# Kernel optimization log

Hardware: AMD Instinct MI355X
Metric: run time of the kernel (lower is better)

The kernel has to match this reference:

```python
import jax, jax.numpy as jnp
from jax import lax
import numpy as np

IMG = 512
NUM_CLASSES = 80
K_PRE = 256            # per-class pre-NMS candidates (TF combined NMS prunes similarly)
MAX_PER_CLASS = 100
MAX_TOTAL = 100
IOU_THR = 0.5
ANY_IOU_THR = 0.7
SCORE_THR = 0.05
NEG = -1e9


def make_anchors(img=IMG):
    """RetinaNet-style anchors for FPN levels 3..7, 9 per cell, [y1,x1,y2,x2]."""
    out = []
    for l in range(3, 8):
        s = 2 ** l
        n = img // s
        c = (np.arange(n) + 0.5) * s
        cy, cx = np.meshgrid(c, c, indexing='ij')
        base = 4.0 * s
        hs, ws = [], []
        for r in [0.5, 1.0, 2.0]:
            for sc in [1.0, 2 ** (1 / 3), 2 ** (2 / 3)]:
                hs.append(base * sc * np.sqrt(r))
                ws.append(base * sc / np.sqrt(r))
        hs = np.asarray(hs); ws = np.asarray(ws)  # [9]
        cy = cy[..., None]; cx = cx[..., None]
        a = np.stack([cy - hs / 2, cx - ws / 2, cy + hs / 2, cx + ws / 2], -1)  # [n,n,9,4]
        out.append(a.reshape(-1, 4))
    return np.concatenate(out, 0).astype(np.float32)


def setup_inputs() -> dict:
    key = jax.random.key(0)
    k1, k2, k3, k4 = jax.random.split(key, 4)
    anchors = jnp.asarray(make_anchors())          # [49104, 4]
    A = anchors.shape[0]
    B = 8
    # logits biased low, mimicking focal-loss bias init; few anchors fire
    y_cls = jax.random.normal(k1, (B, A, NUM_CLASSES), jnp.float32) - 4.0
    y_bbox = jax.random.normal(k2, (B, A, 4), jnp.float32) * 0.1
    orig_hs = jax.random.randint(k3, (B,), 480, 1080).astype(jnp.int32)
    orig_ws = jax.random.randint(k4, (B,), 640, 1920).astype(jnp.int32)
    return {"y_cls": y_cls, "y_bbox": y_bbox, "anchors": anchors,
            "orig_hs": orig_hs, "orig_ws": orig_ws}


def decode_boxes(anchors, rel):
    """bboxes_from_fast_rcnn: anchors [A,4], rel [B,A,4] -> [B,A,4] (y1,x1,y2,x2)."""
    ha = anchors[:, 2] - anchors[:, 0]
    wa = anchors[:, 3] - anchors[:, 1]
    cya = anchors[:, 0] + 0.5 * ha
    cxa = anchors[:, 1] + 0.5 * wa
    cy = cya + rel[..., 0] * ha
    cx = cxa + rel[..., 1] * wa
    h = ha * jnp.exp(rel[..., 2])
    w = wa * jnp.exp(rel[..., 3])
    return jnp.stack([cy - 0.5 * h, cx - 0.5 * w, cy + 0.5 * h, cx + 0.5 * w], -1)


def pairwise_iou(b):
    """[K,4] -> [K,K] IoU."""
    y1, x1, y2, x2 = b[:, 0], b[:, 1], b[:, 2], b[:, 3]
    area = (y2 - y1) * (x2 - x1)
    ih = jnp.maximum(jnp.minimum(y2[:, None], y2[None, :]) - jnp.maximum(y1[:, None], y1[None, :]), 0.0)
    iw = jnp.maximum(jnp.minimum(x2[:, None], x2[None, :]) - jnp.maximum(x1[:, None], x1[None, :]), 0.0)
    inter = ih * iw
    return inter / (area[:, None] + area[None, :] - inter + 1e-8)


def greedy_nms(boxes, valid, iou_thr, max_keep):
    """Greedy NMS over score-sorted boxes [K,4]; returns keep mask [K]."""
    K = boxes.shape[0]
    iou_m = pairwise_iou(boxes)
    ar = jnp.arange(K)

    def step(sup, i):
        k = valid[i] & jnp.logical_not(sup[i])
        sup = sup | (k & (iou_m[i] > iou_thr) & (ar > i))
        return sup, k

    _, keep = lax.scan(step, jnp.zeros(K, bool), ar)
    rank = jnp.cumsum(keep) - 1
    return keep & (rank < max_keep)


def reference(y_cls, y_bbox, anchors, orig_hs, orig_ws):
    B, A, C = y_cls.shape
    scores = jax.nn.sigmoid(y_cls)                 # [B,A,C]
    boxes = decode_boxes(anchors, y_bbox)          # [B,A,4]

    # --- per-class combined NMS ---
    st = jnp.swapaxes(scores, 1, 2)                # [B,C,A]
    top_s, top_i = lax.top_k(st, K_PRE)            # [B,C,K]
    boxes_c = jnp.take_along_axis(boxes[:, None, :, :], top_i[..., None], axis=2)  # [B,C,K,4]
    valid = top_s > SCORE_THR
    keep = jax.vmap(jax.vmap(lambda b, v: greedy_nms(b, v, IOU_THR, MAX_PER_CLASS)))(boxes_c, valid)

    masked = jnp.where(keep, top_s, NEG).reshape(B, -1)           # [B,C*K]
    cls_ids = jnp.broadcast_to(jnp.arange(C, dtype=jnp.float32)[None, :, None],
                               (B, C, K_PRE)).reshape(B, -1)
    boxes_flat = boxes_c.reshape(B, -1, 4)

    sel_s, sel_i = lax.top_k(masked, MAX_TOTAL)    # [B,T]
    sel_valid = sel_s > NEG / 2
    sel_boxes = jnp.take_along_axis(boxes_flat, sel_i[..., None], axis=1)
    sel_cls = jnp.take_along_axis(cls_ids, sel_i, axis=1)
    out_scores = jnp.where(sel_valid, sel_s, 0.0)
    out_boxes = jnp.where(sel_valid[..., None], sel_boxes, 0.0)
    out_cls = jnp.where(sel_valid, sel_cls, 0.0)
    valid_det = jnp.sum(sel_valid, axis=1).astype(jnp.int32)

    # --- resize to original image dims (bboxes_resize) ---
    rh = orig_hs.astype(jnp.float32) / IMG
    rw = orig_ws.astype(jnp.float32) / IMG
    scale = jnp.stack([rh, rw, rh, rw], -1)[:, None, :]
    lim = jnp.stack([orig_hs, orig_ws, orig_hs, orig_ws], -1).astype(jnp.float32)[:, None, :]
    rb = jnp.clip(out_boxes * scale, 0.0, lim)

    # --- class-agnostic second NMS (scores already sorted desc) ---
    v2 = jnp.arange(MAX_TOTAL)[None, :] < valid_det[:, None]
    keep2 = jax.vmap(lambda b, v: greedy_nms(b, v, ANY_IOU_THR, MAX_TOTAL))(rb, v2)

    # compact kept detections to the front (ragged gather in the original)
    perm = jnp.argsort(jnp.logical_not(keep2), axis=1, stable=True)
    fb = jnp.take_along_axis(rb, perm[..., None], axis=1)
    fs = jnp.take_along_axis(out_scores, perm, axis=1)
    fc = jnp.take_along_axis(out_cls, perm, axis=1)
    nv = jnp.sum(keep2, axis=1).astype(jnp.int32)
    m = jnp.arange(MAX_TOTAL)[None, :] < nv[:, None]
    return (jnp.where(m[..., None], fb, 0.0), jnp.where(m, fs, 0.0), jnp.where(m, fc, 0.0), nv)
```

## Files before the change

### kernel.cpp

```cpp
#include <hip/hip_runtime.h>
#include <cstdint>

#define NEGF    (-1.0e9f)
#define THR_PRE (-1.55f)
#define THR_VALID (-2.9444389791664403f)
#define CAP 512
#define FCAP 1024
#define NCLS 80
#define APB 372
#define BCAP 512
#define BLCAP 8192

__device__ __forceinline__ unsigned fkey(float v){
  unsigned b = __float_as_uint(v);
  return b ^ ((b & 0x80000000u) ? 0xFFFFFFFFu : 0x80000000u);
}
__device__ __forceinline__ float fkey_inv(unsigned k){
  unsigned b = (k & 0x80000000u) ? (k ^ 0x80000000u) : ~k;
  return __uint_as_float(b);
}

template<int N, int NT>
__device__ void bitonic_desc(unsigned long long* buf){
  const int tid = threadIdx.x;
  __syncthreads();
  for (int k = 2; k <= N; k <<= 1){
    for (int j = k >> 1; j > 0; j >>= 1){
      for (int t = tid; t < N/2; t += NT){
        int i = ((t & ~(j-1)) << 1) | (t & (j-1));
        int p = i | j;
        unsigned long long a = buf[i], b = buf[p];
        bool sw = ((i & k) == 0) ? (a < b) : (a > b);
        if (sw){ buf[i] = b; buf[p] = a; }
      }
      __syncthreads();
    }
  }
}

__global__ void k_init(unsigned* cnt, int n, unsigned* bcnt, int nb){
  int i = blockIdx.x*blockDim.x + threadIdx.x;
  if (i < n) cnt[i] = 0u;
  if (i < nb) bcnt[i] = 0u;
}

__global__ void k_filter(const float* __restrict__ ycls, int A,
                         unsigned* __restrict__ cnt, unsigned long long* __restrict__ pairs){
  const int b  = blockIdx.y;
  const int a0 = blockIdx.x * APB;
  const int tid = threadIdx.x;
  __shared__ unsigned long long s_cand[BCAP];
  __shared__ unsigned char     s_crow[BCAP];
  __shared__ unsigned s_n;
  __shared__ unsigned s_cnt[NCLS], s_base[NCLS], s_cur[NCLS];
  if (tid == 0) s_n = 0;
  if (tid < NCLS){ s_cnt[tid] = 0u; s_cur[tid] = 0u; }
  __syncthreads();

  const float4* p4 = (const float4*)(ycls + ((size_t)b*A + a0)*NCLS);
  const int nval = (min(APB, A - a0)) * NCLS;
  const int n4 = nval >> 2;
  for (int t = tid; t < n4; t += blockDim.x){
    float4 v = p4[t];
    int idx  = t << 2;
    int aloc = idx / NCLS;
    int c0   = idx - aloc*NCLS;
    unsigned a = (unsigned)(a0 + aloc);
    float vv[4] = {v.x, v.y, v.z, v.w};
    #pragma unroll
    for (int j = 0; j < 4; j++){
      if (vv[j] > THR_PRE){
        unsigned s = atomicAdd(&s_n, 1u);
        if (s < BCAP){
          s_cand[s] = ((unsigned long long)fkey(vv[j]) << 32) | (unsigned)(~a);
          s_crow[s] = (unsigned char)(c0 + j);
        }
      }
    }
  }
  __syncthreads();
  unsigned n = s_n; if (n > BCAP) n = BCAP;
  for (unsigned i = tid; i < n; i += blockDim.x)
    atomicAdd(&s_cnt[s_crow[i]], 1u);
  __syncthreads();
  if (tid < NCLS && s_cnt[tid] > 0u)
    s_base[tid] = atomicAdd(&cnt[b*NCLS + tid], s_cnt[tid]);
  __syncthreads();
  for (unsigned i = tid; i < n; i += blockDim.x){
    int c = s_crow[i];
    unsigned off = s_base[c] + atomicAdd(&s_cur[c], 1u);
    if (off < CAP) pairs[(size_t)(b*NCLS + c)*CAP + off] = s_cand[i];
  }
}

__global__ void k_topk_nms(const unsigned* __restrict__ cnt, const unsigned long long* __restrict__ pairs,
                           const float* __restrict__ ycls, const float4* __restrict__ ybbox,
                           const float4* __restrict__ anchors,
                           float4* __restrict__ sbox,
                           unsigned long long* __restrict__ bcand, unsigned* __restrict__ bcnt,
                           unsigned A, unsigned C){
  const int row = blockIdx.x, tid = threadIdx.x;
  const unsigned b = (unsigned)row / C, c = (unsigned)row % C;
  __shared__ __align__(16) char smem[5120];
  unsigned long long* L = (unsigned long long*)smem;
  __shared__ unsigned s_n;
  __shared__ unsigned long long s_K;
  __shared__ unsigned long long s_keep[4];
  __shared__ unsigned s_kc, s_bbase;

  unsigned long long a, bb;
  unsigned n = cnt[row]; if (n > CAP) n = CAP;
  if (n >= 256u){
    const unsigned long long* pr = pairs + (size_t)row*CAP;
    int i0 = 2*tid, i1 = 2*tid + 1;
    a  = (i0 < (int)n) ? pr[i0] : 0ull;
    bb = (i1 < (int)n) ? pr[i1] : 0ull;
  } else {
    if (tid == 0) s_n = 0;
    __syncthreads();
    for (int i = tid; i < CAP; i += 256) L[i] = 0ull;
    __syncthreads();
    for (unsigned aa = tid; aa < A; aa += 256){
      float v = ycls[((size_t)b*A + aa)*C + c];
      if (v > THR_VALID){
        unsigned s = atomicAdd(&s_n, 1u);
        if (s < CAP) L[s] = ((unsigned long long)fkey(v) << 32) | (unsigned)(~aa);
      }
    }
    __syncthreads();
    n = s_n; if (n > CAP) n = CAP;
    a = L[2*tid]; bb = L[2*tid + 1];
    __syncthreads();
  }

  auto ce_local = [&](int k){
    bool desc = (((2*tid) & k) == 0);
    bool sw = desc ? (a < bb) : (a > bb);
    if (sw){ unsigned long long t = a; a = bb; bb = t; }
  };
  auto ce_shfl = [&](int k, int m){
    unsigned long long pa = __shfl_xor(a, m);
    unsigned long long pb = __shfl_xor(bb, m);
    bool low  = ((tid & m) == 0);
    bool desc = (((2*tid) & k) == 0);
    bool takeMax = (low == desc);
    a  = takeMax ? (a  > pa ? a  : pa) : (a  < pa ? a  : pa);
    bb = takeMax ? (bb > pb ? bb : pb) : (bb < pb ? bb : pb);
  };
  auto ce_lds = [&](int k, int j){
    L[2*tid] = a; L[2*tid + 1] = bb;
    __syncthreads();
    unsigned long long pa = L[(2*tid) ^ j];
    unsigned long long pb = L[(2*tid + 1) ^ j];
    bool lowa = (((2*tid) & j) == 0);
    bool desc = (((2*tid) & k) == 0);
    bool takeMax = (lowa == desc);
    a  = takeMax ? (a  > pa ? a  : pa) : (a  < pa ? a  : pa);
    bb = takeMax ? (bb > pb ? bb : pb) : (bb < pb ? bb : pb);
    __syncthreads();
  };

  ce_local(2);
  #pragma unroll
  for (int k = 4; k <= 128; k <<= 1){
    #pragma unroll
    for (int m = k >> 2; m >= 1; m >>= 1) ce_shfl(k, m);
    ce_local(k);
  }
  ce_lds(256, 128);
  #pragma unroll
  for (int m = 32; m >= 1; m >>= 1) ce_shfl(256, m);
  ce_local(256);
  ce_lds(512, 256);
  ce_lds(512, 128);
  #pragma unroll
  for (int m = 32; m >= 1; m >>= 1) ce_shfl(512, m);
  ce_local(512);

  if (tid < 128){ L[2*tid] = a; L[2*tid + 1] = bb; }
  __syncthreads();
  unsigned long long p = L[tid];
  __syncthreads();

  unsigned m = n < 256u ? n : 256u;
  float lg = NEGF; float4 bx = make_float4(0.f,0.f,0.f,0.f);
  if ((unsigned)tid < m){
    unsigned key = (unsigned)(p >> 32);
    unsigned aidx = ~(unsigned)(p & 0xFFFFFFFFull);
    lg = fkey_inv(key);
    float4 an = anchors[aidx];
    float4 rl = ybbox[(size_t)b*A + aidx];
    float ha = an.z - an.x, wa = an.w - an.y;
    float cya = an.x + 0.5f*ha, cxa = an.y + 0.5f*wa;
    float cy = cya + rl.x*ha, cx = cxa + rl.y*wa;
    float h = ha * expf(rl.z), w = wa * expf(rl.w);
    bx = make_float4(cy - 0.5f*h, cx - 0.5f*w, cy + 0.5f*h, cx + 0.5f*w);
  }
  sbox[(size_t)row*256 + tid] = bx;

  float4* s_box = (float4*)smem;
  float*  s_ar  = (float*)(smem + 4096);
  float AA = (bx.z - bx.x) * (bx.w - bx.y);
  s_box[tid] = bx; s_ar[tid] = AA;
  if (tid == 0) s_kc = 0u;
  __syncthreads();

  unsigned long long M[4];
  float Y1 = bx.x, X1 = bx.y, Y2 = bx.z, X2 = bx.w;
  #pragma unroll
  for (int ch = 0; ch < 4; ++ch){
    unsigned long long mm = 0ull;
    for (int i0 = ch*64; i0 < ch*64 + 64 && i0 < tid; i0 += 4){
      #pragma unroll
      for (int k = 0; k < 4; ++k){
        int i = i0 + k;
        float4 ob = s_box[i];
        float oar = s_ar[i];
        float ih = fmaxf(fminf(Y2, ob.z) - fmaxf(Y1, ob.x), 0.f);
        float iw = fmaxf(fminf(X2, ob.w) - fmaxf(X1, ob.y), 0.f);
        float inter = ih * iw;
        float iou = inter / (AA + oar - inter + 1e-8f);
        if (iou > 0.5f && i < tid) mm |= 1ull << (i & 63);
      }
    }
    M[ch] = mm;
  }

  bool valid = lg > THR_VALID;
  bool sup = false;
  #pragma unroll
  for (int ch = 0; ch < 4; ++ch){
    __syncthreads();
    if ((tid >> 6) == ch){
      unsigned long long S = __ballot(sup);
      unsigned long long V = __ballot(valid);
      unsigned long long Mcc = M[ch];
      unsigned long long kept = 0ull, keep_o = 0ull;
      unsigned kc = s_kc;
      for (int i = 0; i < 64; ++i){
        if (((V >> i) & 1ull) && !((S >> i) & 1ull)){
          if (kc < 100u) keep_o |= 1ull << i;
          kc++;
          kept |= 1ull << i;
          S |= __ballot((Mcc >> i) & 1ull);
        }
      }
      if ((tid & 63) == 0){ s_K = kept; s_keep[ch] = keep_o; s_kc = kc; }
    }
    __syncthreads();
    sup = sup || ((M[ch] & s_K) != 0ull);
  }

  const unsigned ch4 = (unsigned)tid >> 6, ln4 = (unsigned)tid & 63u;
  bool kp = (s_keep[ch4] >> ln4) & 1ull;
  unsigned kt = (unsigned)(__popcll(s_keep[0]) + __popcll(s_keep[1]) +
                           __popcll(s_keep[2]) + __popcll(s_keep[3]));
  if (tid == 0) s_bbase = atomicAdd(&bcnt[b], kt);
  __syncthreads();
  if (kp){
    unsigned pre = (unsigned)__popcll(s_keep[ch4] & ((1ull << ln4) - 1ull));
    for (unsigned k2 = 0; k2 < ch4; ++k2) pre += (unsigned)__popcll(s_keep[k2]);
    unsigned f = c*256u + (unsigned)tid;
    bcand[(size_t)b*BLCAP + s_bbase + pre] =
      ((unsigned long long)fkey(lg) << 32) | (unsigned)(~f);
  }
}

__global__ void k_final(const unsigned long long* __restrict__ bcand, const unsigned* __restrict__ bcnt,
                        const float4* __restrict__ sbox,
                        const int* __restrict__ ohs, const int* __restrict__ ows,
                        float* __restrict__ out, int C, int B){
  const int b = blockIdx.x, tid = threadIdx.x;
  __shared__ unsigned hist[4096];
  __shared__ unsigned nb, thrkey;
  __shared__ unsigned long long buf[FCAP];
  __shared__ float ry1[100],rx1[100],ry2[100],rx2[100],rar[100],rsc[100],rcl[100];
  __shared__ unsigned long long s_K2, s_keep2[2];
  __shared__ unsigned s_kc2;

  const unsigned total = bcnt[b];
  for (int i = tid; i < 4096; i += 1024) hist[i] = 0u;
  if (tid == 0){ nb = 0u; thrkey = 0xFFFFFFFFu; s_kc2 = 0u; }
  __syncthreads();
  const unsigned long long* cb = bcand + (size_t)b*BLCAP;
  for (unsigned i = tid; i < total; i += 1024)
    atomicAdd(&hist[(unsigned)(cb[i] >> 32) >> 20], 1u);
  __syncthreads();

  const unsigned target = total < 100u ? total : 100u;
  if (tid < 64 && target > 0u){
    const int ln = tid;
    unsigned v = 0;
    #pragma unroll 8
    for (int i = 0; i < 64; i++) v += hist[(ln << 6) | ((i + ln) & 63)];
    #pragma unroll
    for (int d = 1; d < 64; d <<= 1){ unsigned u = __shfl_down(v, d); if (ln + d < 64) v += u; }
    unsigned long long gm = __ballot(v >= target);
    int gstar = 63 - __builtin_clzll(gm);
    unsigned ca = (gstar < 63) ? __shfl(v, gstar + 1) : 0u;
    unsigned h = hist[(gstar << 6) | ln];
    #pragma unroll
    for (int d = 1; d < 64; d <<= 1){ unsigned u = __shfl_down(h, d); if (ln + d < 64) h += u; }
    h += ca;
    unsigned long long bm = __ballot(h >= target);
    int bstar = 63 - __builtin_clzll(bm);
    if (ln == 0) thrkey = (unsigned)((gstar << 6) | bstar) << 20;
  }
  __syncthreads();
  const unsigned tk = thrkey;
  if (tk != 0xFFFFFFFFu){
    for (unsigned i = tid; i < total; i += 1024){
      unsigned long long e = cb[i];
      if ((unsigned)(e >> 32) >= tk){
        unsigned sl = atomicAdd(&nb, 1u);
        if (sl < FCAP) buf[sl] = e;
      }
    }
  }
  __syncthreads();
  unsigned nbv = nb; if (nbv > FCAP) nbv = FCAP;
  for (int i = tid; i < FCAP; i += 1024) if (i >= (int)nbv) buf[i] = 0ull;
  bitonic_desc<FCAP,1024>(buf);
  const int vd = (int)target;

  if (tid < 100){
    float e0=0,e1=0,e2=0,e3=0, s=0, cl=0;
    if (tid < vd){
      unsigned long long p = buf[tid];
      unsigned key = (unsigned)(p >> 32);
      unsigned f   = ~(unsigned)(p & 0xFFFFFFFFull);
      float lg = fkey_inv(key);
      s  = 1.0f / (1.0f + expf(-lg));
      int c = (int)(f >> 8), kk = (int)(f & 255u);
      cl = (float)c;
      float4 bx = sbox[((size_t)(b*C + c))*256 + kk];
      float oh = (float)ohs[b], ow = (float)ows[b];
      float rh = oh / 512.0f, rw = ow / 512.0f;
      e0 = fminf(fmaxf(bx.x*rh, 0.f), oh);
      e1 = fminf(fmaxf(bx.y*rw, 0.f), ow);
      e2 = fminf(fmaxf(bx.z*rh, 0.f), oh);
      e3 = fminf(fmaxf(bx.w*rw, 0.f), ow);
    }
    ry1[tid]=e0; rx1[tid]=e1; ry2[tid]=e2; rx2[tid]=e3;
    rar[tid]=(e2-e0)*(e3-e1); rsc[tid]=s; rcl[tid]=cl;
  }
  __syncthreads();

  unsigned long long M2[2] = {0ull, 0ull};
  if (tid < 100){
    float Y1=ry1[tid],X1=rx1[tid],Y2=ry2[tid],X2=rx2[tid],AA=rar[tid];
    for (int i = 0; i < tid; i++){
      float ih = fmaxf(fminf(Y2,ry2[i]) - fmaxf(Y1,ry1[i]), 0.f);
      float iw = fmaxf(fminf(X2,rx2[i]) - fmaxf(X1,rx1[i]), 0.f);
      float inter = ih*iw;
      float iou = inter / (AA + rar[i] - inter + 1e-8f);
      if (iou > 0.7f){ if (i < 64) M2[0] |= 1ull<<i; else M2[1] |= 1ull<<(i-64); }
    }
  }
  bool valid2 = tid < vd;
  bool sup2 = false;
  #pragma unroll
  for (int ch = 0; ch < 2; ++ch){
    __syncthreads();
    if ((tid >> 6) == ch){
      unsigned long long S = __ballot(sup2);
      unsigned long long V = __ballot(valid2);
      unsigned long long Mcc = M2[ch];
      unsigned long long kept = 0ull, keep_o = 0ull;
      unsigned kc = s_kc2;
      for (int i = 0; i < 64; ++i){
        if (((V >> i) & 1ull) && !((S >> i) & 1ull)){
          if (kc < 100u) keep_o |= 1ull << i;
          kc++;
          kept |= 1ull << i;
          S |= __ballot((Mcc >> i) & 1ull);
        }
      }
      if ((tid & 63) == 0){ s_K2 = kept; s_keep2[ch] = keep_o; s_kc2 = kc; }
    }
    __syncthreads();
    if (tid < 128) sup2 = sup2 || ((M2[ch] & s_K2) != 0ull);
  }

  float* fb  = out;
  float* fs  = out + (size_t)B*100*4;
  float* fc  = fs + (size_t)B*100;
  float* fnv = fc + (size_t)B*100;
  if (tid < 100){
    fs[b*100 + tid] = 0.f; fc[b*100 + tid] = 0.f;
    ((float4*)fb)[b*100 + tid] = make_float4(0.f,0.f,0.f,0.f);
  }
  __syncthreads();
  if (tid < 100){
    unsigned ch = (unsigned)tid >> 6, ln = (unsigned)tid & 63u;
    bool kp = (s_keep2[ch] >> ln) & 1ull;
    if (kp){
      unsigned pos = (unsigned)__popcll(s_keep2[ch] & ((1ull << ln) - 1ull));
      if (ch) pos += (unsigned)__popcll(s_keep2[0]);
      fs[b*100 + pos] = rsc[tid];
      fc[b*100 + pos] = rcl[tid];
      ((float4*)fb)[b*100 + pos] = make_float4(ry1[tid], rx1[tid], ry2[tid], rx2[tid]);
    }
  }
  if (tid == 0) fnv[b] = (float)(__popcll(s_keep2[0]) + __popcll(s_keep2[1]));
}

extern "C" void kernel_launch(void* const* d_in, const int* in_sizes, int n_in,
                              void* d_out, int out_size, void* d_ws, size_t ws_size,
                              hipStream_t stream){
  const float* ycls    = (const float*)d_in[0];
  const float* ybbox   = (const float*)d_in[1];
  const float* anchors = (const float*)d_in[2];
  const int*   ohs     = (const int*)d_in[3];
  const int*   ows     = (const int*)d_in[4];
  const int A = in_sizes[2] / 4;
  const int B = in_sizes[3];
  const int C = in_sizes[0] / (A * B);
  const int R = B * C;

  char* ws = (char*)d_ws;
  unsigned*            cnt   = (unsigned*)ws;
  unsigned long long*  pairs = (unsigned long long*)(ws + 4096);
  float4*              sbox  = (float4*)(ws + 4096 + (size_t)R*CAP*8);
  unsigned long long*  bcand = (unsigned long long*)(ws + 4096 + (size_t)R*CAP*8 + (size_t)R*256*16);
  unsigned*            bcnt  = (unsigned*)(ws + 4096 + (size_t)R*CAP*8 + (size_t)R*256*16 + (size_t)B*BLCAP*8);

  const int S = (A + APB - 1) / APB;
  k_init     <<<1, 1024, 0, stream>>>(cnt, R, bcnt, B);
  k_filter   <<<dim3(S, B), 256, 0, stream>>>(ycls, A, cnt, pairs);
  k_topk_nms <<<R, 256, 0, stream>>>(cnt, pairs, ycls, (const float4*)ybbox, (const float4*)anchors,
                                     sbox, bcand, bcnt, (unsigned)A, (unsigned)C);
  k_final    <<<B, 1024, 0, stream>>>(bcand, bcnt, sbox, ohs, ows, (float*)d_out, C, B);
}
```

Baseline: 129.3 us.

## Spread NMS IoU mask build over 1024 threads with tiled 64x64 blocks

Launches the per-class top-k/NMS kernel with 1024 threads. The sort still runs on the first 256 threads, while the IoU suppression matrix is split into 64x64 tiles, one wavefront per upper-triangular tile, so each thread computes 64 comparisons instead of up to 256. The suppression state now lives in shared-memory masks instead of per-thread registers. An early-out comparison skips the division when IoU cannot exceed the threshold. APB in the filter kernel also drops from 372 to 256, giving more filter blocks. In exchange, the 1024-thread blocks sit mostly idle during the sort and serial greedy scan, and a __syncthreads call inside the divergent tid<256 branch is risky.

```diff
diff --git a/kernel.cpp b/kernel.cpp
--- a/kernel.cpp
+++ b/kernel.cpp
@@ -7,7 +7,7 @@
 #define CAP 512
 #define FCAP 1024
 #define NCLS 80
-#define APB 372
+#define APB 256
 #define BCAP 512
 #define BLCAP 8192
 
@@ -93,7 +93,8 @@
   }
 }
 
-__global__ void k_topk_nms(const unsigned* __restrict__ cnt, const unsigned long long* __restrict__ pairs,
+__global__ __launch_bounds__(1024) void k_topk_nms(
+                           const unsigned* __restrict__ cnt, const unsigned long long* __restrict__ pairs,
                            const float* __restrict__ ycls, const float4* __restrict__ ybbox,
                            const float4* __restrict__ anchors,
                            float4* __restrict__ sbox,
@@ -103,24 +104,24 @@
   const unsigned b = (unsigned)row / C, c = (unsigned)row % C;
   __shared__ __align__(16) char smem[5120];
   unsigned long long* L = (unsigned long long*)smem;
-  __shared__ unsigned s_n;
-  __shared__ unsigned long long s_K;
-  __shared__ unsigned long long s_keep[4];
-  __shared__ unsigned s_kc, s_bbase;
-
-  unsigned long long a, bb;
+  __shared__ unsigned s_n, s_kc, s_bbase;
+  __shared__ unsigned long long s_K, s_keep[4], s_valmask[4], s_supmask[4];
+
+  unsigned long long a = 0ull, bb = 0ull;
   unsigned n = cnt[row]; if (n > CAP) n = CAP;
   if (n >= 256u){
-    const unsigned long long* pr = pairs + (size_t)row*CAP;
-    int i0 = 2*tid, i1 = 2*tid + 1;
-    a  = (i0 < (int)n) ? pr[i0] : 0ull;
-    bb = (i1 < (int)n) ? pr[i1] : 0ull;
+    if (tid < 256){
+      const unsigned long long* pr = pairs + (size_t)row*CAP;
+      int i0 = 2*tid;
+      a  = (i0   < (int)n) ? pr[i0]   : 0ull;
+      bb = (i0+1 < (int)n) ? pr[i0+1] : 0ull;
+    }
   } else {
     if (tid == 0) s_n = 0;
     __syncthreads();
-    for (int i = tid; i < CAP; i += 256) L[i] = 0ull;
-    __syncthreads();
-    for (unsigned aa = tid; aa < A; aa += 256){
+    for (int i = tid; i < CAP; i += 1024) L[i] = 0ull;
+    __syncthreads();
+    for (unsigned aa = tid; aa < A; aa += 1024){
       float v = ycls[((size_t)b*A + aa)*C + c];
       if (v > THR_VALID){
         unsigned s = atomicAdd(&s_n, 1u);
@@ -129,7 +130,7 @@
     }
     __syncthreads();
     n = s_n; if (n > CAP) n = CAP;
-    a = L[2*tid]; bb = L[2*tid + 1];
+    if (tid < 256){ a = L[2*tid]; bb = L[2*tid + 1]; }
     __syncthreads();
   }
 
@@ -147,9 +148,8 @@
     a  = takeMax ? (a  > pa ? a  : pa) : (a  < pa ? a  : pa);
     bb = takeMax ? (bb > pb ? bb : pb) : (bb < pb ? bb : pb);
   };
-  auto ce_lds = [&](int k, int j){
-    L[2*tid] = a; L[2*tid + 1] = bb;
-    __syncthreads();
+  auto st = [&](){ L[2*tid] = a; L[2*tid + 1] = bb; };
+  auto ld_merge = [&](int k, int j){
     unsigned long long pa = L[(2*tid) ^ j];
     unsigned long long pb = L[(2*tid + 1) ^ j];
     bool lowa = (((2*tid) & j) == 0);
@@ -157,35 +157,48 @@
     bool takeMax = (lowa == desc);
     a  = takeMax ? (a  > pa ? a  : pa) : (a  < pa ? a  : pa);
     bb = takeMax ? (bb > pb ? bb : pb) : (bb < pb ? bb : pb);
-    __syncthreads();
   };
 
-  ce_local(2);
-  #pragma unroll
-  for (int k = 4; k <= 128; k <<= 1){
-    #pragma unroll
-    for (int m = k >> 2; m >= 1; m >>= 1) ce_shfl(k, m);
-    ce_local(k);
-  }
-  ce_lds(256, 128);
-  #pragma unroll
-  for (int m = 32; m >= 1; m >>= 1) ce_shfl(256, m);
-  ce_local(256);
-  ce_lds(512, 256);
-  ce_lds(512, 128);
-  #pragma unroll
-  for (int m = 32; m >= 1; m >>= 1) ce_shfl(512, m);
-  ce_local(512);
-
+  if (tid < 256){
+    ce_local(2);
+    #pragma unroll
+    for (int k = 4; k <= 128; k <<= 1){
+      #pragma unroll
+      for (int m = k >> 2; m >= 1; m >>= 1) ce_shfl(k, m);
+      ce_local(k);
+    }
+    st();
+  }
+  __syncthreads();
+  if (tid < 256) ld_merge(256, 128);
+  __syncthreads();
+  if (tid < 256){
+    #pragma unroll
+    for (int m = 32; m >= 1; m >>= 1) ce_shfl(256, m);
+    ce_local(256);
+    st();
+  }
+  __syncthreads();
+  if (tid < 256) ld_merge(512, 256);
+  __syncthreads();
+  if (tid < 256) st();
+  __syncthreads();
+  if (tid < 256) ld_merge(512, 128);
+  __syncthreads();
+  if (tid < 256){
+    #pragma unroll
+    for (int m = 32; m >= 1; m >>= 1) ce_shfl(512, m);
+    ce_local(512);
+  }
   if (tid < 128){ L[2*tid] = a; L[2*tid + 1] = bb; }
   __syncthreads();
-  unsigned long long p = L[tid];
+  unsigned long long p = (tid < 256) ? L[tid] : 0ull;
   __syncthreads();
 
   unsigned m = n < 256u ? n : 256u;
   float lg = NEGF; float4 bx = make_float4(0.f,0.f,0.f,0.f);
   if ((unsigned)tid < m){
-    unsigned key = (unsigned)(p >> 32);
+    unsigned key  = (unsigned)(p >> 32);
     unsigned aidx = ~(unsigned)(p & 0xFFFFFFFFull);
     lg = fkey_inv(key);
     float4 an = anchors[aidx];
@@ -196,45 +209,52 @@
     float h = ha * expf(rl.z), w = wa * expf(rl.w);
     bx = make_float4(cy - 0.5f*h, cx - 0.5f*w, cy + 0.5f*h, cx + 0.5f*w);
   }
-  sbox[(size_t)row*256 + tid] = bx;
 
   float4* s_box = (float4*)smem;
   float*  s_ar  = (float*)(smem + 4096);
-  float AA = (bx.z - bx.x) * (bx.w - bx.y);
-  s_box[tid] = bx; s_ar[tid] = AA;
+  if (tid < 256){
+    sbox[(size_t)row*256 + tid] = bx;
+    float AA = (bx.z - bx.x) * (bx.w - bx.y);
+    s_box[tid] = bx; s_ar[tid] = AA;
+    unsigned long long vm = __ballot(lg > THR_VALID);
+    if ((tid & 63) == 0) s_valmask[tid >> 6] = vm;
+  }
+  if (tid < 4) s_supmask[tid] = 0ull;
   if (tid == 0) s_kc = 0u;
   __syncthreads();
 
-  unsigned long long M[4];
-  float Y1 = bx.x, X1 = bx.y, Y2 = bx.z, X2 = bx.w;
-  #pragma unroll
-  for (int ch = 0; ch < 4; ++ch){
-    unsigned long long mm = 0ull;
-    for (int i0 = ch*64; i0 < ch*64 + 64 && i0 < tid; i0 += 4){
+  const int w  = tid >> 6;
+  const int q  = w >> 2, pp = w & 3;
+  const int col = (pp << 6) | (tid & 63);
+  float4 cb = s_box[col];
+  float cAA = s_ar[col];
+  unsigned long long Mp = 0ull;
+  if (q <= pp){
+    const int i0 = q << 6;
+    for (int i = i0; i < i0 + 64; i += 4){
       #pragma unroll
       for (int k = 0; k < 4; ++k){
-        int i = i0 + k;
-        float4 ob = s_box[i];
-        float oar = s_ar[i];
-        float ih = fmaxf(fminf(Y2, ob.z) - fmaxf(Y1, ob.x), 0.f);
-        float iw = fmaxf(fminf(X2, ob.w) - fmaxf(X1, ob.y), 0.f);
+        int ii = i + k;
+        float4 ob = s_box[ii];
+        float oar = s_ar[ii];
+        float ih = fmaxf(fminf(cb.z, ob.z) - fmaxf(cb.x, ob.x), 0.f);
+        float iw = fmaxf(fminf(cb.w, ob.w) - fmaxf(cb.y, ob.y), 0.f);
         float inter = ih * iw;
-        float iou = inter / (AA + oar - inter + 1e-8f);
-        if (iou > 0.5f && i < tid) mm |= 1ull << (i & 63);
-      }
-    }
-    M[ch] = mm;
-  }
-
-  bool valid = lg > THR_VALID;
-  bool sup = false;
-  #pragma unroll
+        float denom = cAA + oar - inter + 1e-8f;
+        if (inter + inter >= 0.999f * denom){
+          float iou = inter / denom;
+          if (iou > 0.5f && ii < col) Mp |= 1ull << (ii & 63);
+        }
+      }
+    }
+  }
+
   for (int ch = 0; ch < 4; ++ch){
     __syncthreads();
-    if ((tid >> 6) == ch){
-      unsigned long long S = __ballot(sup);
-      unsigned long long V = __ballot(valid);
-      unsigned long long Mcc = M[ch];
+    if (w == 5*ch){
+      unsigned long long S = s_supmask[ch];
+      unsigned long long V = s_valmask[ch];
+      unsigned long long Mcc = Mp;
       unsigned long long kept = 0ull, keep_o = 0ull;
       unsigned kc = s_kc;
       for (int i = 0; i < 64; ++i){
@@ -248,21 +268,30 @@
       if ((tid & 63) == 0){ s_K = kept; s_keep[ch] = keep_o; s_kc = kc; }
     }
     __syncthreads();
-    sup = sup || ((M[ch] & s_K) != 0ull);
-  }
-
-  const unsigned ch4 = (unsigned)tid >> 6, ln4 = (unsigned)tid & 63u;
-  bool kp = (s_keep[ch4] >> ln4) & 1ull;
-  unsigned kt = (unsigned)(__popcll(s_keep[0]) + __popcll(s_keep[1]) +
-                           __popcll(s_keep[2]) + __popcll(s_keep[3]));
-  if (tid == 0) s_bbase = atomicAdd(&bcnt[b], kt);
-  __syncthreads();
-  if (kp){
-    unsigned pre = (unsigned)__popcll(s_keep[ch4] & ((1ull << ln4) - 1ull));
-    for (unsigned k2 = 0; k2 < ch4; ++k2) pre += (unsigned)__popcll(s_keep[k2]);
-    unsigned f = c*256u + (unsigned)tid;
-    bcand[(size_t)b*BLCAP + s_bbase + pre] =
-      ((unsigned long long)fkey(lg) << 32) | (unsigned)(~f);
+    if (q == ch){
+      bool hit = (Mp & s_K) != 0ull;
+      unsigned long long hm = __ballot(hit);
+      if ((tid & 63) == 0) s_supmask[pp] |= hm;
+    }
+  }
+  __syncthreads();
+
+  if (tid < 256){
+    const unsigned ch4 = (unsigned)tid >> 6, ln4 = (unsigned)tid & 63u;
+    bool kp = (s_keep[ch4] >> ln4) & 1ull;
+    unsigned kt = (unsigned)(__popcll(s_keep[0]) + __popcll(s_keep[1]) +
+                             __popcll(s_keep[2]) + __popcll(s_keep[3]));
+    if (tid == 0) s_bbase = atomicAdd(&bcnt[b], kt);
+    __syncthreads();
+    if (kp){
+      unsigned pre = (unsigned)__popcll(s_keep[ch4] & ((1ull << ln4) - 1ull));
+      for (unsigned k2 = 0; k2 < ch4; ++k2) pre += (unsigned)__popcll(s_keep[k2]);
+      unsigned f = c*256u + (unsigned)tid;
+      bcand[(size_t)b*BLCAP + s_bbase + pre] =
+        ((unsigned long long)fkey(lg) << 32) | (unsigned)(~f);
+    }
+  } else {
+    __syncthreads();
   }
 }
 
@@ -428,7 +457,7 @@
   const int S = (A + APB - 1) / APB;
   k_init     <<<1, 1024, 0, stream>>>(cnt, R, bcnt, B);
   k_filter   <<<dim3(S, B), 256, 0, stream>>>(ycls, A, cnt, pairs);
-  k_topk_nms <<<R, 256, 0, stream>>>(cnt, pairs, ycls, (const float4*)ybbox, (const float4*)anchors,
-                                     sbox, bcand, bcnt, (unsigned)A, (unsigned)C);
+  k_topk_nms <<<R, 1024, 0, stream>>>(cnt, pairs, ycls, (const float4*)ybbox, (const float4*)anchors,
+                                      sbox, bcand, bcnt, (unsigned)A, (unsigned)C);
   k_final    <<<B, 1024, 0, stream>>>(bcand, bcnt, sbox, ohs, ows, (float*)d_out, C, B);
 }
```

Measured after the change: 142.5 us. +10.2%, slower.

## Replace global atomic candidate appends with per-shard slots and prefix scans

Applied to the files above, without the earlier changes.

The filter kernel now writes per-shard per-class candidate counts and fixed-size slots instead of global atomics, which removes the init kernel launch and the contended global atomics. The top-k kernel gathers the slots with a shared-memory prefix scan. The NMS kernel writes kept candidates per row, and the final kernel reads them with per-class counts instead of a global atomic base. The change also enlarges the anchors per block and adds a cheap IoU pre-check that skips the division, at the cost of capping candidates per shard at 20, which may drop candidates for dense classes.

```diff
diff --git a/kernel.cpp b/kernel.cpp
--- a/kernel.cpp
+++ b/kernel.cpp
@@ -7,9 +7,11 @@
 #define CAP 512
 #define FCAP 1024
 #define NCLS 80
-#define APB 372
+#define APB 512
+#define NSH 96
+#define SLOT 20
 #define BCAP 512
-#define BLCAP 8192
+#define KCAP 128
 
 __device__ __forceinline__ unsigned fkey(float v){
   unsigned b = __float_as_uint(v);
@@ -38,21 +40,16 @@
   }
 }
 
-__global__ void k_init(unsigned* cnt, int n, unsigned* bcnt, int nb){
-  int i = blockIdx.x*blockDim.x + threadIdx.x;
-  if (i < n) cnt[i] = 0u;
-  if (i < nb) bcnt[i] = 0u;
-}
-
 __global__ void k_filter(const float* __restrict__ ycls, int A,
-                         unsigned* __restrict__ cnt, unsigned long long* __restrict__ pairs){
+                         unsigned* __restrict__ pcnt, unsigned long long* __restrict__ pairs){
   const int b  = blockIdx.y;
-  const int a0 = blockIdx.x * APB;
+  const int sh = blockIdx.x;
+  const int a0 = sh * APB;
   const int tid = threadIdx.x;
   __shared__ unsigned long long s_cand[BCAP];
   __shared__ unsigned char     s_crow[BCAP];
   __shared__ unsigned s_n;
-  __shared__ unsigned s_cnt[NCLS], s_base[NCLS], s_cur[NCLS];
+  __shared__ unsigned s_cnt[NCLS], s_cur[NCLS];
   if (tid == 0) s_n = 0;
   if (tid < NCLS){ s_cnt[tid] = 0u; s_cur[tid] = 0u; }
   __syncthreads();
@@ -83,42 +80,61 @@
   for (unsigned i = tid; i < n; i += blockDim.x)
     atomicAdd(&s_cnt[s_crow[i]], 1u);
   __syncthreads();
-  if (tid < NCLS && s_cnt[tid] > 0u)
-    s_base[tid] = atomicAdd(&cnt[b*NCLS + tid], s_cnt[tid]);
-  __syncthreads();
+  if (tid < NCLS){
+    unsigned ccl = s_cnt[tid]; if (ccl > SLOT) ccl = SLOT;
+    pcnt[(size_t)(b*NCLS + tid)*NSH + sh] = ccl;
+  }
   for (unsigned i = tid; i < n; i += blockDim.x){
     int c = s_crow[i];
-    unsigned off = s_base[c] + atomicAdd(&s_cur[c], 1u);
-    if (off < CAP) pairs[(size_t)(b*NCLS + c)*CAP + off] = s_cand[i];
-  }
-}
-
-__global__ void k_topk_nms(const unsigned* __restrict__ cnt, const unsigned long long* __restrict__ pairs,
+    unsigned off = atomicAdd(&s_cur[c], 1u);
+    if (off < SLOT)
+      pairs[((size_t)(b*NCLS + c)*NSH + sh)*SLOT + off] = s_cand[i];
+  }
+}
+
+__global__ void k_topk_nms(const unsigned* __restrict__ pcnt, const unsigned long long* __restrict__ pairs,
                            const float* __restrict__ ycls, const float4* __restrict__ ybbox,
                            const float4* __restrict__ anchors,
                            float4* __restrict__ sbox,
-                           unsigned long long* __restrict__ bcand, unsigned* __restrict__ bcnt,
+                           unsigned long long* __restrict__ bcand, unsigned* __restrict__ kcnt,
                            unsigned A, unsigned C){
   const int row = blockIdx.x, tid = threadIdx.x;
   const unsigned b = (unsigned)row / C, c = (unsigned)row % C;
   __shared__ __align__(16) char smem[5120];
   unsigned long long* L = (unsigned long long*)smem;
-  __shared__ unsigned s_n;
-  __shared__ unsigned long long s_K;
-  __shared__ unsigned long long s_keep[4];
-  __shared__ unsigned s_kc, s_bbase;
-
-  unsigned long long a, bb;
-  unsigned n = cnt[row]; if (n > CAP) n = CAP;
+  __shared__ unsigned sc[128];
+  __shared__ unsigned s_n, s_kc;
+  __shared__ unsigned long long s_K, s_keep[4];
+
+  unsigned ct = 0;
+  if (tid < 128){
+    ct = (tid < NSH) ? pcnt[(size_t)row*NSH + tid] : 0u;
+    sc[tid] = ct;
+  }
+  __syncthreads();
+  #pragma unroll
+  for (int d = 1; d < 128; d <<= 1){
+    unsigned v = 0;
+    if (tid < 128 && tid >= d) v = sc[tid - d];
+    __syncthreads();
+    if (tid < 128 && tid >= d) sc[tid] += v;
+    __syncthreads();
+  }
+  unsigned n = sc[127];
+
+  for (int i = tid; i < CAP; i += 256) L[i] = 0ull;
+  __syncthreads();
   if (n >= 256u){
-    const unsigned long long* pr = pairs + (size_t)row*CAP;
-    int i0 = 2*tid, i1 = 2*tid + 1;
-    a  = (i0 < (int)n) ? pr[i0] : 0ull;
-    bb = (i1 < (int)n) ? pr[i1] : 0ull;
+    if (tid < NSH && ct > 0){
+      unsigned base = sc[tid] - ct;
+      const unsigned long long* src = pairs + ((size_t)row*NSH + tid)*SLOT;
+      for (unsigned i = 0; i < ct; ++i){
+        unsigned d = base + i;
+        if (d < CAP) L[d] = src[i];
+      }
+    }
   } else {
     if (tid == 0) s_n = 0;
-    __syncthreads();
-    for (int i = tid; i < CAP; i += 256) L[i] = 0ull;
     __syncthreads();
     for (unsigned aa = tid; aa < A; aa += 256){
       float v = ycls[((size_t)b*A + aa)*C + c];
@@ -128,10 +144,11 @@
       }
     }
     __syncthreads();
-    n = s_n; if (n > CAP) n = CAP;
-    a = L[2*tid]; bb = L[2*tid + 1];
-    __syncthreads();
-  }
+    n = s_n;
+  }
+  if (n > CAP) n = CAP;
+  __syncthreads();
+  unsigned long long a = L[2*tid], bb = L[2*tid + 1];
 
   auto ce_local = [&](int k){
     bool desc = (((2*tid) & k) == 0);
@@ -185,7 +202,7 @@
   unsigned m = n < 256u ? n : 256u;
   float lg = NEGF; float4 bx = make_float4(0.f,0.f,0.f,0.f);
   if ((unsigned)tid < m){
-    unsigned key = (unsigned)(p >> 32);
+    unsigned key  = (unsigned)(p >> 32);
     unsigned aidx = ~(unsigned)(p & 0xFFFFFFFFull);
     lg = fkey_inv(key);
     float4 an = anchors[aidx];
@@ -219,8 +236,11 @@
         float ih = fmaxf(fminf(Y2, ob.z) - fmaxf(Y1, ob.x), 0.f);
         float iw = fmaxf(fminf(X2, ob.w) - fmaxf(X1, ob.y), 0.f);
         float inter = ih * iw;
-        float iou = inter / (AA + oar - inter + 1e-8f);
-        if (iou > 0.5f && i < tid) mm |= 1ull << (i & 63);
+        float denom = AA + oar - inter + 1e-8f;
+        if (inter + inter >= 0.999f * denom){
+          float iou = inter / denom;
+          if (iou > 0.5f && i < tid) mm |= 1ull << (i & 63);
+        }
       }
     }
     M[ch] = mm;
@@ -253,39 +273,44 @@
 
   const unsigned ch4 = (unsigned)tid >> 6, ln4 = (unsigned)tid & 63u;
   bool kp = (s_keep[ch4] >> ln4) & 1ull;
-  unsigned kt = (unsigned)(__popcll(s_keep[0]) + __popcll(s_keep[1]) +
+  if (tid == 0)
+    kcnt[row] = (unsigned)(__popcll(s_keep[0]) + __popcll(s_keep[1]) +
                            __popcll(s_keep[2]) + __popcll(s_keep[3]));
-  if (tid == 0) s_bbase = atomicAdd(&bcnt[b], kt);
-  __syncthreads();
   if (kp){
     unsigned pre = (unsigned)__popcll(s_keep[ch4] & ((1ull << ln4) - 1ull));
     for (unsigned k2 = 0; k2 < ch4; ++k2) pre += (unsigned)__popcll(s_keep[k2]);
     unsigned f = c*256u + (unsigned)tid;
-    bcand[(size_t)b*BLCAP + s_bbase + pre] =
+    bcand[(size_t)row*KCAP + pre] =
       ((unsigned long long)fkey(lg) << 32) | (unsigned)(~f);
   }
 }
 
-__global__ void k_final(const unsigned long long* __restrict__ bcand, const unsigned* __restrict__ bcnt,
+__global__ void k_final(const unsigned long long* __restrict__ bcand, const unsigned* __restrict__ kcnt,
                         const float4* __restrict__ sbox,
                         const int* __restrict__ ohs, const int* __restrict__ ows,
                         float* __restrict__ out, int C, int B){
   const int b = blockIdx.x, tid = threadIdx.x;
   __shared__ unsigned hist[4096];
-  __shared__ unsigned nb, thrkey;
+  __shared__ unsigned kc[NCLS];
+  __shared__ unsigned s_total, nb, thrkey;
   __shared__ unsigned long long buf[FCAP];
   __shared__ float ry1[100],rx1[100],ry2[100],rx2[100],rar[100],rsc[100],rcl[100];
   __shared__ unsigned long long s_K2, s_keep2[2];
   __shared__ unsigned s_kc2;
 
-  const unsigned total = bcnt[b];
   for (int i = tid; i < 4096; i += 1024) hist[i] = 0u;
-  if (tid == 0){ nb = 0u; thrkey = 0xFFFFFFFFu; s_kc2 = 0u; }
-  __syncthreads();
-  const unsigned long long* cb = bcand + (size_t)b*BLCAP;
-  for (unsigned i = tid; i < total; i += 1024)
-    atomicAdd(&hist[(unsigned)(cb[i] >> 32) >> 20], 1u);
-  __syncthreads();
+  if (tid < NCLS) kc[tid] = kcnt[b*NCLS + tid];
+  if (tid == 0){ s_total = 0u; nb = 0u; thrkey = 0xFFFFFFFFu; s_kc2 = 0u; }
+  __syncthreads();
+  if (tid < NCLS) atomicAdd(&s_total, kc[tid]);
+  const unsigned long long* cb = bcand + (size_t)(b*NCLS)*KCAP;
+  for (int t = tid; t < NCLS*KCAP; t += 1024){
+    int cc = t >> 7, i = t & (KCAP-1);
+    if ((unsigned)i < kc[cc])
+      atomicAdd(&hist[(unsigned)(cb[(size_t)cc*KCAP + i] >> 32) >> 20], 1u);
+  }
+  __syncthreads();
+  const unsigned total = s_total;
 
   const unsigned target = total < 100u ? total : 100u;
   if (tid < 64 && target > 0u){
@@ -309,11 +334,14 @@
   __syncthreads();
   const unsigned tk = thrkey;
   if (tk != 0xFFFFFFFFu){
-    for (unsigned i = tid; i < total; i += 1024){
-      unsigned long long e = cb[i];
-      if ((unsigned)(e >> 32) >= tk){
-        unsigned sl = atomicAdd(&nb, 1u);
-        if (sl < FCAP) buf[sl] = e;
+    for (int t = tid; t < NCLS*KCAP; t += 1024){
+      int cc = t >> 7, i = t & (KCAP-1);
+      if ((unsigned)i < kc[cc]){
+        unsigned long long e = cb[(size_t)cc*KCAP + i];
+        if ((unsigned)(e >> 32) >= tk){
+          unsigned sl = atomicAdd(&nb, 1u);
+          if (sl < FCAP) buf[sl] = e;
+        }
       }
     }
   }
@@ -367,16 +395,16 @@
       unsigned long long V = __ballot(valid2);
       unsigned long long Mcc = M2[ch];
       unsigned long long kept = 0ull, keep_o = 0ull;
-      unsigned kc = s_kc2;
+      unsigned kc2 = s_kc2;
       for (int i = 0; i < 64; ++i){
         if (((V >> i) & 1ull) && !((S >> i) & 1ull)){
-          if (kc < 100u) keep_o |= 1ull << i;
-          kc++;
+          if (kc2 < 100u) keep_o |= 1ull << i;
+          kc2++;
           kept |= 1ull << i;
           S |= __ballot((Mcc >> i) & 1ull);
         }
       }
-      if ((tid & 63) == 0){ s_K2 = kept; s_keep2[ch] = keep_o; s_kc2 = kc; }
+      if ((tid & 63) == 0){ s_K2 = kept; s_keep2[ch] = keep_o; s_kc2 = kc2; }
     }
     __syncthreads();
     if (tid < 128) sup2 = sup2 || ((M2[ch] & s_K2) != 0ull);
@@ -419,16 +447,15 @@
   const int R = B * C;
 
   char* ws = (char*)d_ws;
-  unsigned*            cnt   = (unsigned*)ws;
-  unsigned long long*  pairs = (unsigned long long*)(ws + 4096);
-  float4*              sbox  = (float4*)(ws + 4096 + (size_t)R*CAP*8);
-  unsigned long long*  bcand = (unsigned long long*)(ws + 4096 + (size_t)R*CAP*8 + (size_t)R*256*16);
-  unsigned*            bcnt  = (unsigned*)(ws + 4096 + (size_t)R*CAP*8 + (size_t)R*256*16 + (size_t)B*BLCAP*8);
+  unsigned*            pcnt  = (unsigned*)ws;
+  unsigned long long*  pairs = (unsigned long long*)(ws + 262144);
+  float4*              sbox  = (float4*)(ws + 262144 + 9830400);
+  unsigned long long*  bcand = (unsigned long long*)(ws + 262144 + 9830400 + 2621440);
+  unsigned*            kcnt  = (unsigned*)(ws + 262144 + 9830400 + 2621440 + 655360);
 
   const int S = (A + APB - 1) / APB;
-  k_init     <<<1, 1024, 0, stream>>>(cnt, R, bcnt, B);
-  k_filter   <<<dim3(S, B), 256, 0, stream>>>(ycls, A, cnt, pairs);
-  k_topk_nms <<<R, 256, 0, stream>>>(cnt, pairs, ycls, (const float4*)ybbox, (const float4*)anchors,
-                                     sbox, bcand, bcnt, (unsigned)A, (unsigned)C);
-  k_final    <<<B, 1024, 0, stream>>>(bcand, bcnt, sbox, ohs, ows, (float*)d_out, C, B);
-}
+  k_filter   <<<dim3(S, B), 256, 0, stream>>>(ycls, A, pcnt, pairs);
+  k_topk_nms <<<R, 256, 0, stream>>>(pcnt, pairs, ycls, (const float4*)ybbox, (const float4*)anchors,
+                                     sbox, bcand, kcnt, (unsigned)A, (unsigned)C);
+  k_final    <<<B, 1024, 0, stream>>>(bcand, kcnt, sbox, ohs, ows, (float*)d_out, C, B);
+}
```

Measured after the change: 137.4 us. 6.2% more time.
